# Optimization experiments

Hardware: AMD Instinct MI355X
Metric: run time of the kernel (lower is better)

Reference implementation:

```python
import jax, jax.numpy as jnp
import numpy as np

EPS = 1e-6
DROP_RATE = 0.25

def setup_inputs() -> dict:
    key = jax.random.key(0)
    k1, k2, k3 = jax.random.split(key, 3)
    B, S, D = 4, 2048, 2048
    inputs = jax.random.normal(k1, (B, S, D), dtype=jnp.float32)
    # keras 'uniform' initializer: U(-0.05, 0.05)
    W_1 = jax.random.uniform(k2, (D, D), dtype=jnp.float32, minval=-0.05, maxval=0.05)
    W_2 = jax.random.uniform(k3, (D, D), dtype=jnp.float32, minval=-0.05, maxval=0.05)
    return {"inputs": inputs, "W_1": W_1, "W_2": W_2}

def reference(inputs, W_1, W_2):
    # LayerNorm over last axis (no affine: gamma/beta unused in original call)
    mean = jnp.mean(inputs, axis=-1, keepdims=True)
    var = jnp.mean(jnp.square(inputs - mean), axis=-1, keepdims=True)
    x_norm = (inputs - mean) / jnp.sqrt(var + EPS)          # [B,S,D]
    # 2-layer MLP with relu
    h = jax.nn.relu(jnp.einsum('bsd,de->bse', x_norm, W_1))  # [B,S,D]
    y = jnp.einsum('bsd,de->bse', h, W_2)                    # [B,S,D]
    # dropout(0.25), inverted scaling, fixed key for determinism
    keep = jax.random.bernoulli(jax.random.key(1), 1.0 - DROP_RATE, y.shape)
    y_drop = jnp.where(keep, y / (1.0 - DROP_RATE), 0.0)
    return x_norm + y_drop
```

## Files before the change

kernel.cpp:

```cpp
#include <hip/hip_runtime.h>
#include <hip/hip_bf16.h>
#include <stdint.h>

#define M_DIM 8192
#define N_DIM 2048
#define K_DIM 2048

typedef __bf16 bf16x8_t __attribute__((ext_vector_type(8)));
typedef float f32x4_t __attribute__((ext_vector_type(4)));

__device__ __forceinline__ unsigned tf_rotl(unsigned x, int r) {
  return (x << r) | (x >> (32 - r));
}
__device__ __forceinline__ unsigned threefry_mask_bits(unsigned ctr) {
  unsigned x0 = 0u, x1 = ctr;
  const unsigned ks0 = 0u, ks1 = 1u, ks2 = 0x1BD11BDBu;
  x0 += ks0; x1 += ks1;
#define TFR(r) { x0 += x1; x1 = tf_rotl(x1, (r)); x1 ^= x0; }
  TFR(13) TFR(15) TFR(26) TFR(6)
  x0 += ks1; x1 += ks2 + 1u;
  TFR(17) TFR(29) TFR(16) TFR(24)
  x0 += ks2; x1 += ks0 + 2u;
  TFR(13) TFR(15) TFR(26) TFR(6)
  x0 += ks0; x1 += ks1 + 3u;
  TFR(17) TFR(29) TFR(16) TFR(24)
  x0 += ks1; x1 += ks2 + 4u;
  TFR(13) TFR(15) TFR(26) TFR(6)
  x0 += ks2; x1 += ks0 + 5u;
#undef TFR
  return x0 ^ x1;
}

__device__ __forceinline__ void gload_lds16(const __hip_bfloat16* g, unsigned short* l) {
  __builtin_amdgcn_global_load_lds(
      (const __attribute__((address_space(1))) unsigned int*)g,
      (__attribute__((address_space(3))) unsigned int*)l,
      16, 0, 0);
}

__global__ __launch_bounds__(256) void wt_kernel(
    const float* __restrict__ W1, const float* __restrict__ W2,
    __hip_bfloat16* __restrict__ W1t, __hip_bfloat16* __restrict__ W2t) {
  __shared__ float tile[32][33];
  const float* src = blockIdx.z ? W2 : W1;
  __hip_bfloat16* dst = blockIdx.z ? W2t : W1t;
  int x = blockIdx.x * 32 + threadIdx.x;
  int y = blockIdx.y * 32 + threadIdx.y;
#pragma unroll
  for (int i = 0; i < 32; i += 8)
    tile[threadIdx.y + i][threadIdx.x] = src[(size_t)(y + i) * N_DIM + x];
  __syncthreads();
  int xo = blockIdx.y * 32 + threadIdx.x;
  int yo = blockIdx.x * 32 + threadIdx.y;
#pragma unroll
  for (int i = 0; i < 32; i += 8)
    dst[(size_t)(yo + i) * K_DIM + xo] = __float2bfloat16(tile[threadIdx.x][threadIdx.y + i]);
}

__global__ __launch_bounds__(256) void ln_kernel(const float* __restrict__ X,
                                                 __hip_bfloat16* __restrict__ Xn) {
  const int row = blockIdx.x;
  const float4* xv = (const float4*)(X + (size_t)row * K_DIM);
  float4 v0 = xv[threadIdx.x];
  float4 v1 = xv[threadIdx.x + 256];
  float s  = v0.x + v0.y + v0.z + v0.w + v1.x + v1.y + v1.z + v1.w;
  float ss = v0.x*v0.x + v0.y*v0.y + v0.z*v0.z + v0.w*v0.w
           + v1.x*v1.x + v1.y*v1.y + v1.z*v1.z + v1.w*v1.w;
#pragma unroll
  for (int off = 32; off > 0; off >>= 1) {
    s  += __shfl_xor(s, off);
    ss += __shfl_xor(ss, off);
  }
  __shared__ float rs[4], rss[4];
  const int wave = threadIdx.x >> 6;
  if ((threadIdx.x & 63) == 0) { rs[wave] = s; rss[wave] = ss; }
  __syncthreads();
  float S  = rs[0] + rs[1] + rs[2] + rs[3];
  float SS = rss[0] + rss[1] + rss[2] + rss[3];
  float mean = S * (1.0f / 2048.0f);
  float var  = SS * (1.0f / 2048.0f) - mean * mean;
  float rstd = 1.0f / sqrtf(var + 1e-6f);
  float vv[8] = {v0.x, v0.y, v0.z, v0.w, v1.x, v1.y, v1.z, v1.w};
  unsigned short o[8];
#pragma unroll
  for (int i = 0; i < 8; i++) {
    __hip_bfloat16 b = __float2bfloat16((vv[i] - mean) * rstd);
    o[i] = *(unsigned short*)&b;
  }
  ushort4* dst = (ushort4*)(Xn + (size_t)row * K_DIM);
  dst[threadIdx.x]       = make_ushort4(o[0], o[1], o[2], o[3]);
  dst[threadIdx.x + 256] = make_ushort4(o[4], o[5], o[6], o[7]);
}

template <int EPI>
__global__ __launch_bounds__(256) void gemm128(
    const __hip_bfloat16* __restrict__ A,
    const __hip_bfloat16* __restrict__ Bt,
    const __hip_bfloat16* __restrict__ Xn,
    __hip_bfloat16* __restrict__ Hout,
    float* __restrict__ Fout) {
  __shared__ unsigned short As[2][128 * 32];
  __shared__ unsigned short Bs[2][128 * 32];
  const int tid  = threadIdx.x;
  const int lane = tid & 63;
  const int wave = tid >> 6;
  const int wm = wave >> 1, wn = wave & 1;
  const int mBase = blockIdx.x * 128;
  const int nBase = blockIdx.y * 128;

  f32x4_t acc[4][4];
#pragma unroll
  for (int i = 0; i < 4; i++)
#pragma unroll
    for (int j = 0; j < 4; j++) acc[i][j] = (f32x4_t){0.f, 0.f, 0.f, 0.f};

  const int r4 = lane >> 2;
  const int c4 = (lane & 3) << 3;
  const __hip_bfloat16* a0 = A  + (size_t)(mBase + 16 * wave       + r4) * K_DIM + c4;
  const __hip_bfloat16* a1 = A  + (size_t)(mBase + 16 * (wave + 4) + r4) * K_DIM + c4;
  const __hip_bfloat16* b0 = Bt + (size_t)(nBase + 16 * wave       + r4) * K_DIM + c4;
  const __hip_bfloat16* b1 = Bt + (size_t)(nBase + 16 * (wave + 4) + r4) * K_DIM + c4;
  const int sOff0 = (16 * wave) * 32;
  const int sOff1 = (16 * (wave + 4)) * 32;

  const int fr = lane & 15;
  const int fq = lane >> 4;
  const int rdOffA = (wm * 64 + fr) * 32 + fq * 8;
  const int rdOffB = (wn * 64 + fr) * 32 + fq * 8;

#define STAGE(buf, k0)                              \
  {                                                 \
    gload_lds16(a0 + (k0), &As[buf][sOff0]);        \
    gload_lds16(a1 + (k0), &As[buf][sOff1]);        \
    gload_lds16(b0 + (k0), &Bs[buf][sOff0]);        \
    gload_lds16(b1 + (k0), &Bs[buf][sOff1]);        \
  }

#define COMPUTE(buf)                                                            \
  {                                                                             \
    bf16x8_t af[4], bfr[4];                                                     \
    _Pragma("unroll")                                                           \
    for (int i = 0; i < 4; i++) af[i]  = *(const bf16x8_t*)(&As[buf][rdOffA] + i * 16 * 32); \
    _Pragma("unroll")                                                           \
    for (int i = 0; i < 4; i++) bfr[i] = *(const bf16x8_t*)(&Bs[buf][rdOffB] + i * 16 * 32); \
    _Pragma("unroll")                                                           \
    for (int mi = 0; mi < 4; mi++)                                              \
      _Pragma("unroll")                                                         \
      for (int ni = 0; ni < 4; ni++)                                            \
        acc[mi][ni] = __builtin_amdgcn_mfma_f32_16x16x32_bf16(af[mi], bfr[ni], acc[mi][ni], 0, 0, 0); \
  }

  STAGE(0, 0)
  for (int k0 = 0; k0 < K_DIM; k0 += 64) {
    __syncthreads();
    if (k0 + 32 < K_DIM) STAGE(1, k0 + 32)
    COMPUTE(0)
    __syncthreads();
    if (k0 + 64 < K_DIM) STAGE(0, k0 + 64)
    COMPUTE(1)
  }
#undef STAGE
#undef COMPUTE

  const int mRow = mBase + wm * 64;
  const int nCol = nBase + wn * 64;
#pragma unroll
  for (int mi = 0; mi < 4; mi++) {
#pragma unroll
    for (int ni = 0; ni < 4; ni++) {
      const int n  = nCol + ni * 16 + fr;
      const int m0 = mRow + mi * 16 + fq * 4;
#pragma unroll
      for (int r = 0; r < 4; r++) {
        float v = acc[mi][ni][r];
        size_t j = (size_t)(m0 + r) * N_DIM + n;
        if (EPI == 0) {
          Hout[j] = __float2bfloat16(fmaxf(v, 0.0f));
        } else {
          unsigned bits = threefry_mask_bits((unsigned)j);
          float y  = (bits < 0xC0000000u) ? v * (1.0f / 0.75f) : 0.0f;
          Fout[j]  = __bfloat162float(Xn[j]) + y;
        }
      }
    }
  }
}

extern "C" void kernel_launch(void* const* d_in, const int* in_sizes, int n_in,
                              void* d_out, int out_size, void* d_ws, size_t ws_size,
                              hipStream_t stream) {
  (void)in_sizes; (void)n_in; (void)out_size; (void)ws_size;
  const float* X  = (const float*)d_in[0];
  const float* W1 = (const float*)d_in[1];
  const float* W2 = (const float*)d_in[2];
  float* out = (float*)d_out;

  unsigned char* ws = (unsigned char*)d_ws;
  __hip_bfloat16* Xn  = (__hip_bfloat16*)(ws);
  __hip_bfloat16* H   = (__hip_bfloat16*)(ws + ((size_t)32 << 20));
  __hip_bfloat16* W1t = (__hip_bfloat16*)(ws + ((size_t)64 << 20));
  __hip_bfloat16* W2t = (__hip_bfloat16*)(ws + ((size_t)72 << 20));

  wt_kernel<<<dim3(64, 64, 2), dim3(32, 8, 1), 0, stream>>>(W1, W2, W1t, W2t);
  ln_kernel<<<M_DIM, 256, 0, stream>>>(X, Xn);
  gemm128<0><<<dim3(M_DIM / 128, N_DIM / 128), 256, 0, stream>>>(Xn, W1t, nullptr, H, nullptr);
  gemm128<1><<<dim3(M_DIM / 128, N_DIM / 128), 256, 0, stream>>>(H, W2t, Xn, nullptr, out);
}
```

Baseline: 363.1 us.

## Double GEMM K-tile to 64 with XOR-swizzled LDS layout

Raises the K depth of each LDS stage from 32 to 64, halving the number of barriers per K loop, and applies an XOR swizzle on the 16-byte column chunks so the fragment reads from the 128-byte LDS rows avoid bank conflicts. The loop is restructured so the final stage is peeled rather than guarded by conditionals. LDS use doubles to 64 KB per block, which may reduce how many blocks fit on a CU.

Result: faster. 319.8 us (-11.9%).

```diff
diff --git a/kernel.cpp b/kernel.cpp
--- a/kernel.cpp
+++ b/kernel.cpp
@@ -99,8 +99,8 @@
     const __hip_bfloat16* __restrict__ Xn,
     __hip_bfloat16* __restrict__ Hout,
     float* __restrict__ Fout) {
-  __shared__ unsigned short As[2][128 * 32];
-  __shared__ unsigned short Bs[2][128 * 32];
+  __shared__ unsigned short As[2][128 * 64];
+  __shared__ unsigned short Bs[2][128 * 64];
   const int tid  = threadIdx.x;
   const int lane = tid & 63;
   const int wave = tid >> 6;
@@ -114,53 +114,68 @@
 #pragma unroll
     for (int j = 0; j < 4; j++) acc[i][j] = (f32x4_t){0.f, 0.f, 0.f, 0.f};
 
-  const int r4 = lane >> 2;
-  const int c4 = (lane & 3) << 3;
-  const __hip_bfloat16* a0 = A  + (size_t)(mBase + 16 * wave       + r4) * K_DIM + c4;
-  const __hip_bfloat16* a1 = A  + (size_t)(mBase + 16 * (wave + 4) + r4) * K_DIM + c4;
-  const __hip_bfloat16* b0 = Bt + (size_t)(nBase + 16 * wave       + r4) * K_DIM + c4;
-  const __hip_bfloat16* b1 = Bt + (size_t)(nBase + 16 * (wave + 4) + r4) * K_DIM + c4;
-  const int sOff0 = (16 * wave) * 32;
-  const int sOff1 = (16 * (wave + 4)) * 32;
+  const int rowIn  = lane >> 3;
+  const int csrc   = ((lane & 7) ^ (rowIn & 7)) << 3;
+  const __hip_bfloat16* aSrc[4];
+  const __hip_bfloat16* bSrc[4];
+  int sDst[4];
+#pragma unroll
+  for (int j = 0; j < 4; j++) {
+    const int ca = wave + 4 * j;
+    aSrc[j] = A  + (size_t)(mBase + 8 * ca + rowIn) * K_DIM + csrc;
+    bSrc[j] = Bt + (size_t)(nBase + 8 * ca + rowIn) * K_DIM + csrc;
+    sDst[j] = ca * 512;
+  }
 
   const int fr = lane & 15;
   const int fq = lane >> 4;
-  const int rdOffA = (wm * 64 + fr) * 32 + fq * 8;
-  const int rdOffB = (wn * 64 + fr) * 32 + fq * 8;
-
-#define STAGE(buf, k0)                              \
-  {                                                 \
-    gload_lds16(a0 + (k0), &As[buf][sOff0]);        \
-    gload_lds16(a1 + (k0), &As[buf][sOff1]);        \
-    gload_lds16(b0 + (k0), &Bs[buf][sOff0]);        \
-    gload_lds16(b1 + (k0), &Bs[buf][sOff1]);        \
-  }
-
-#define COMPUTE(buf)                                                            \
+  const int sw = fr & 7;
+  const int cA0 = (fq ^ sw) * 8;
+  const int cA1 = ((4 | fq) ^ sw) * 8;
+  const int rowOffA = (wm * 64 + fr) * 64;
+  const int rowOffB = (wn * 64 + fr) * 64;
+
+#define STAGE(buf, k0)                                        \
+  {                                                           \
+    _Pragma("unroll")                                         \
+    for (int j = 0; j < 4; j++) {                             \
+      gload_lds16(aSrc[j] + (k0), &As[buf][sDst[j]]);         \
+      gload_lds16(bSrc[j] + (k0), &Bs[buf][sDst[j]]);         \
+    }                                                         \
+  }
+
+#define COMPUTE_HALF(buf, cOff)                                                 \
   {                                                                             \
     bf16x8_t af[4], bfr[4];                                                     \
     _Pragma("unroll")                                                           \
-    for (int i = 0; i < 4; i++) af[i]  = *(const bf16x8_t*)(&As[buf][rdOffA] + i * 16 * 32); \
+    for (int i = 0; i < 4; i++) af[i]  = *(const bf16x8_t*)(&As[buf][rowOffA + i * 1024 + (cOff)]); \
     _Pragma("unroll")                                                           \
-    for (int i = 0; i < 4; i++) bfr[i] = *(const bf16x8_t*)(&Bs[buf][rdOffB] + i * 16 * 32); \
+    for (int i = 0; i < 4; i++) bfr[i] = *(const bf16x8_t*)(&Bs[buf][rowOffB + i * 1024 + (cOff)]); \
     _Pragma("unroll")                                                           \
     for (int mi = 0; mi < 4; mi++)                                              \
       _Pragma("unroll")                                                         \
       for (int ni = 0; ni < 4; ni++)                                            \
         acc[mi][ni] = __builtin_amdgcn_mfma_f32_16x16x32_bf16(af[mi], bfr[ni], acc[mi][ni], 0, 0, 0); \
   }
+#define COMPUTE(buf) { COMPUTE_HALF(buf, cA0) COMPUTE_HALF(buf, cA1) }
 
   STAGE(0, 0)
-  for (int k0 = 0; k0 < K_DIM; k0 += 64) {
+  for (int k0 = 0; k0 < K_DIM - 128; k0 += 128) {
     __syncthreads();
-    if (k0 + 32 < K_DIM) STAGE(1, k0 + 32)
+    STAGE(1, k0 + 64)
     COMPUTE(0)
     __syncthreads();
-    if (k0 + 64 < K_DIM) STAGE(0, k0 + 64)
+    STAGE(0, k0 + 128)
     COMPUTE(1)
   }
+  __syncthreads();
+  STAGE(1, K_DIM - 64)
+  COMPUTE(0)
+  __syncthreads();
+  COMPUTE(1)
 #undef STAGE
 #undef COMPUTE
+#undef COMPUTE_HALF
 
   const int mRow = mBase + wm * 64;
   const int nCol = nBase + wn * 64;
```
